# Performance work log

Measured on AMD Instinct MI355X. Metric: run time of the kernel, lower is better.

Reference implementation:

```python
import jax, jax.numpy as jnp
import numpy as np

ATT = 32      # att_size per spatial dim (pooled grid is 32x32, N=1024)
HEADS = 8

def _pool_sum(x, out):
    # adaptive max + adaptive avg pool (exact uniform windows since W%out==0)
    B, C, W, H = x.shape
    kw, kh = W // out, H // out
    r = x.reshape(B, C, out, kw, out, kh)
    return r.max(axis=(3, 5)) + r.mean(axis=(3, 5))

def _lerp_axis(x, out_len, axis):
    in_len = x.shape[axis]
    pos = jnp.arange(out_len, dtype=x.dtype) * ((in_len - 1) / (out_len - 1))
    i0 = jnp.floor(pos).astype(jnp.int32)
    i1 = jnp.minimum(i0 + 1, in_len - 1)
    t = pos - i0.astype(x.dtype)
    shp = [1] * x.ndim
    shp[axis] = out_len
    t = t.reshape(shp)
    return jnp.take(x, i0, axis=axis) * (1 - t) + jnp.take(x, i1, axis=axis) * t

def _upsample_bilinear_ac(x, out_h, out_w):
    # bilinear, align_corners=True (separable)
    return _lerp_axis(_lerp_axis(x, out_h, 2), out_w, 3)

def setup_inputs() -> dict:
    key = jax.random.key(0)
    k1, k2, k3, k4 = jax.random.split(key, 4)
    B, C, W, H = 8, 256, 128, 128
    input1 = jax.random.normal(k1, (B, C, W, H), dtype=jnp.float32)
    input2 = jax.random.normal(k2, (B, C // 2, W, H), dtype=jnp.float32)
    # 1x1 conv: out=C, in=C//2 (kaiming-ish scale)
    conv_w = jax.random.normal(k3, (C, C // 2), dtype=jnp.float32) * (1.0 / np.sqrt(C // 2))
    conv_b = jax.random.normal(k4, (C,), dtype=jnp.float32) * 0.01
    return {"input1": input1, "input2": input2, "conv_w": conv_w, "conv_b": conv_b}

def reference(input1, input2, conv_w, conv_b):
    B, C, W, H = input1.shape
    # channel projection (1x1 conv) since input2 has C//2 channels
    x2 = jnp.einsum('bihw,oi->bohw', input2, conv_w) + conv_b[None, :, None, None]
    p1 = _pool_sum(input1, ATT)   # [B,C,32,32]
    p2 = _pool_sum(x2, ATT)
    N = ATT * ATT
    q = p1.reshape(B, C, N).transpose(2, 0, 1)  # [N,B,C]
    k = p2.reshape(B, C, N).transpose(2, 0, 1)
    v = k
    scale = 1.0 / np.sqrt(C // HEADS)
    w = jnp.einsum('nbc,nec->nbe', q, k)        # [N,B,B]
    w = jax.nn.softmax(w * scale, axis=-1)
    a = jnp.einsum('nbe,nec->nbc', w, v)        # [N,B,C]
    attn = a.transpose(1, 2, 0).reshape(B, C, ATT, ATT)
    up = _upsample_bilinear_ac(attn, W, H)
    return jax.nn.sigmoid(up)
```

## Files before the change

kernel.cpp:

```cpp
#include <hip/hip_runtime.h>
#include <math.h>

namespace {

constexpr int Bn = 8, Cn = 256, CIN = 128, Wd = 128, Hd = 128, ATTn = 32, Nn = ATTn * ATTn;

typedef __attribute__((ext_vector_type(8))) short short8;
typedef __attribute__((ext_vector_type(4))) float f32x4;

__device__ inline unsigned short bf16_rne(float f) {
    unsigned int u = __float_as_uint(f);
    unsigned int r = (u + 0x7FFFu + ((u >> 16) & 1u)) >> 16;
    return (unsigned short)r;
}

__device__ inline int fsw(int px) { return (px ^ (px >> 3)) & 7; }

__global__ __launch_bounds__(256) void pool1_kernel(const float* __restrict__ in1,
                                                    float* __restrict__ p1t) {
    __shared__ float tile[32 * 9];
    const int t = threadIdx.x;
    const int bid = blockIdx.x;
    const int cg = bid & 31, oy = (bid >> 5) & 31, b = bid >> 10;
    const int c = t >> 5, ox = t & 31;

    const float* src = in1 + (((size_t)(b * Cn + cg * 8 + c) * Wd) + oy * 4) * Hd + ox * 4;
    f32x4 r0 = *reinterpret_cast<const f32x4*>(src);
    f32x4 r1 = *reinterpret_cast<const f32x4*>(src + Hd);
    f32x4 r2 = *reinterpret_cast<const f32x4*>(src + 2 * Hd);
    f32x4 r3 = *reinterpret_cast<const f32x4*>(src + 3 * Hd);

    float mx = fmaxf(fmaxf(fmaxf(r0[0], r0[1]), fmaxf(r0[2], r0[3])),
                     fmaxf(fmaxf(r1[0], r1[1]), fmaxf(r1[2], r1[3])));
    mx = fmaxf(mx, fmaxf(fmaxf(fmaxf(r2[0], r2[1]), fmaxf(r2[2], r2[3])),
                         fmaxf(fmaxf(r3[0], r3[1]), fmaxf(r3[2], r3[3]))));
    float sm = ((r0[0] + r0[1]) + (r0[2] + r0[3])) + ((r1[0] + r1[1]) + (r1[2] + r1[3]))
             + ((r2[0] + r2[1]) + (r2[2] + r2[3])) + ((r3[0] + r3[1]) + (r3[2] + r3[3]));

    tile[ox * 9 + c] = mx + sm * (1.f / 16.f);
    __syncthreads();

    const int ox2 = t >> 3, c2 = t & 7;
    p1t[((size_t)b * Nn + oy * 32 + ox2) * Cn + cg * 8 + c2] = tile[ox2 * 9 + c2];
}

__global__ __launch_bounds__(512, 4) void convpool_kernel(const float* __restrict__ in2,
                                                          const float* __restrict__ cw,
                                                          const float* __restrict__ cb,
                                                          float* __restrict__ p2t) {
    __shared__ __align__(16) unsigned char smem[32768];

    const int t = threadIdx.x;
    const int w = t >> 6;
    const int l = t & 63;
    const int bid2 = blockIdx.x;
    const int b = bid2 >> 7;
    const int r = bid2 & 127;
    const int oy = r >> 2, xq = r & 3;

    f32x4 ra[2][4];
    int x4v[2], rowv[2], k4v[2];
#pragma unroll
    for (int h = 0; h < 2; ++h) {
        const int i = t + h * 512;
        x4v[h] = i & 7; rowv[h] = (i >> 3) & 3; k4v[h] = i >> 5;
        const float* p = in2 + ((size_t)(b * CIN + k4v[h] * 4) * Wd + oy * 4 + rowv[h]) * Hd
                         + xq * 32 + x4v[h] * 4;
#pragma unroll
        for (int kk2 = 0; kk2 < 4; ++kk2)
            ra[h][kk2] = *reinterpret_cast<const f32x4*>(p + (size_t)kk2 * Wd * Hd);
    }

    const int n_lo = l & 15;
    const int khi = l >> 4;
    short8 bfrag[2][4];
#pragma unroll
    for (int f = 0; f < 2; ++f) {
        const int n = w * 32 + f * 16 + n_lo;
#pragma unroll
        for (int kk = 0; kk < 4; ++kk) {
            const float* wp = cw + n * CIN + kk * 32 + khi * 8;
            f32x4 va = *reinterpret_cast<const f32x4*>(wp);
            f32x4 vb = *reinterpret_cast<const f32x4*>(wp + 4);
            short8 s;
            s[0] = (short)bf16_rne(va[0]); s[1] = (short)bf16_rne(va[1]);
            s[2] = (short)bf16_rne(va[2]); s[3] = (short)bf16_rne(va[3]);
            s[4] = (short)bf16_rne(vb[0]); s[5] = (short)bf16_rne(vb[1]);
            s[6] = (short)bf16_rne(vb[2]); s[7] = (short)bf16_rne(vb[3]);
            bfrag[f][kk] = s;
        }
    }
    const float bias2_0 = 2.f * cb[w * 32 + n_lo];
    const float bias2_1 = 2.f * cb[w * 32 + 16 + n_lo];

#pragma unroll
    for (int h = 0; h < 2; ++h) {
#pragma unroll
        for (int j = 0; j < 4; ++j) {
            const int px = x4v[h] * 16 + rowv[h] * 4 + j;
            uint2 u;
            u.x = (unsigned int)bf16_rne(ra[h][0][j]) | ((unsigned int)bf16_rne(ra[h][1][j]) << 16);
            u.y = (unsigned int)bf16_rne(ra[h][2][j]) | ((unsigned int)bf16_rne(ra[h][3][j]) << 16);
            const int off = px * 256 + ((k4v[h] * 8) ^ (fsw(px) << 4));
            *reinterpret_cast<uint2*>(smem + off) = u;
        }
    }
    __syncthreads();

#pragma unroll
    for (int cl = 0; cl < 8; ++cl) {
        f32x4 acc0 = {0.f, 0.f, 0.f, 0.f};
        f32x4 acc1 = {0.f, 0.f, 0.f, 0.f};
        const int px = cl * 16 + n_lo;
        const int sw = fsw(px) << 4;
#pragma unroll
        for (int kk = 0; kk < 4; ++kk) {
            short8 a = *reinterpret_cast<const short8*>(
                smem + px * 256 + ((kk * 64 + khi * 16) ^ sw));
            acc0 = __builtin_amdgcn_mfma_f32_16x16x32_bf16(a, bfrag[0][kk], acc0, 0, 0, 0);
            acc1 = __builtin_amdgcn_mfma_f32_16x16x32_bf16(a, bfrag[1][kk], acc1, 0, 0, 0);
        }
        float mx0 = fmaxf(fmaxf(acc0[0], acc0[1]), fmaxf(acc0[2], acc0[3]));
        float sm0 = (acc0[0] + acc0[1]) + (acc0[2] + acc0[3]);
        float mx1 = fmaxf(fmaxf(acc1[0], acc1[1]), fmaxf(acc1[2], acc1[3]));
        float sm1 = (acc1[0] + acc1[1]) + (acc1[2] + acc1[3]);
        mx0 = fmaxf(mx0, __shfl_xor(mx0, 16)); sm0 += __shfl_xor(sm0, 16);
        mx0 = fmaxf(mx0, __shfl_xor(mx0, 32)); sm0 += __shfl_xor(sm0, 32);
        mx1 = fmaxf(mx1, __shfl_xor(mx1, 16)); sm1 += __shfl_xor(sm1, 16);
        mx1 = fmaxf(mx1, __shfl_xor(mx1, 32)); sm1 += __shfl_xor(sm1, 32);
        if (l < 16) {
            const int cell = oy * 32 + xq * 8 + cl;
            float* dst = p2t + ((size_t)b * Nn + cell) * Cn + w * 32 + n_lo;
            dst[0]  = mx0 + sm0 * (1.f / 16.f) + bias2_0;
            dst[16] = mx1 + sm1 * (1.f / 16.f) + bias2_1;
        }
    }
}

__global__ __launch_bounds__(256) void attn_kernel(const float* __restrict__ p1t,
                                                   const float* __restrict__ p2t,
                                                   float* __restrict__ att) {
    __shared__ float q[Bn][260];
    __shared__ float kk[Bn][260];
    __shared__ float wsm[Bn][8];
    const int n = blockIdx.x, t = threadIdx.x;

#pragma unroll
    for (int i = 0; i < 2; ++i) {
        const int f = t + i * 256;
        const int bb = f >> 6, cq = f & 63;
        const size_t off = ((size_t)bb * Nn + n) * Cn + cq * 4;
        *reinterpret_cast<float4*>(&q[bb][cq * 4])  = *reinterpret_cast<const float4*>(p1t + off);
        *reinterpret_cast<float4*>(&kk[bb][cq * 4]) = *reinterpret_cast<const float4*>(p2t + off);
    }
    __syncthreads();

    {
        const int chunk = t & 3, pair = t >> 2;
        const int e = pair & 7, bb = pair >> 3;
        float s = 0.f;
#pragma unroll
        for (int i = 0; i < 64; ++i)
            s = fmaf(q[bb][i * 4 + chunk], kk[e][i * 4 + chunk], s);
        s += __shfl_xor(s, 1);
        s += __shfl_xor(s, 2);
        s *= 0.17677669529663687f;
        float m = fmaxf(s, __shfl_xor(s, 4));
        m = fmaxf(m, __shfl_xor(m, 8));
        m = fmaxf(m, __shfl_xor(m, 16));
        float p = __expf(s - m);
        float d = p + __shfl_xor(p, 4);
        d += __shfl_xor(d, 8);
        d += __shfl_xor(d, 16);
        if (chunk == 0) wsm[bb][e] = p / d;
    }
    __syncthreads();

    float kv[8];
#pragma unroll
    for (int e = 0; e < 8; ++e) kv[e] = kk[e][t];
#pragma unroll
    for (int bb = 0; bb < 8; ++bb) {
        float s = 0.f;
#pragma unroll
        for (int e = 0; e < 8; ++e) s = fmaf(wsm[bb][e], kv[e], s);
        att[((size_t)bb * Cn + t) * Nn + n] = s;
    }
}

__global__ __launch_bounds__(256) void upsample_kernel(const float* __restrict__ att,
                                                       float* __restrict__ out) {
    __shared__ float tile[ATTn * ATTn];
    int bc = blockIdx.x, t = threadIdx.x;
    reinterpret_cast<float4*>(tile)[t] =
        reinterpret_cast<const float4*>(att + (size_t)bc * Nn)[t];
    __syncthreads();

    int tx = t & 31, ty = t >> 5;
    int xi0[4], xi1[4];
    float xt[4];
#pragma unroll
    for (int j = 0; j < 4; ++j) {
        int x = tx * 4 + j;
        float pos = (float)x * (31.f / 127.f);
        int i0 = (int)pos;
        xi0[j] = i0;
        xi1[j] = min(i0 + 1, 31);
        xt[j] = pos - (float)i0;
    }

    for (int r = 0; r < 16; ++r) {
        int y = ty + r * 8;
        float posy = (float)y * (31.f / 127.f);
        int y0 = (int)posy;
        int y1 = min(y0 + 1, 31);
        float ft = posy - (float)y0;
        float o_[4];
#pragma unroll
        for (int j = 0; j < 4; ++j) {
            float v00 = tile[y0 * 32 + xi0[j]];
            float v01 = tile[y0 * 32 + xi1[j]];
            float v10 = tile[y1 * 32 + xi0[j]];
            float v11 = tile[y1 * 32 + xi1[j]];
            float top = v00 * (1.f - ft) + v10 * ft;
            float bot = v01 * (1.f - ft) + v11 * ft;
            float val = top * (1.f - xt[j]) + bot * xt[j];
            o_[j] = 1.f / (1.f + __expf(-val));
        }
        *reinterpret_cast<float4*>(out + ((size_t)bc * Wd + y) * Hd + tx * 4) =
            make_float4(o_[0], o_[1], o_[2], o_[3]);
    }
}

}

extern "C" void kernel_launch(void* const* d_in, const int* in_sizes, int n_in,
                              void* d_out, int out_size, void* d_ws, size_t ws_size,
                              hipStream_t stream) {
    const float* input1 = (const float*)d_in[0];
    const float* input2 = (const float*)d_in[1];
    const float* conv_w = (const float*)d_in[2];
    const float* conv_b = (const float*)d_in[3];
    float* out = (float*)d_out;

    float* p1t = (float*)d_ws;
    float* p2t = p1t + (size_t)Bn * Cn * Nn;
    float* att = p2t + (size_t)Bn * Cn * Nn;

    pool1_kernel<<<dim3(8192), dim3(256), 0, stream>>>(input1, p1t);
    convpool_kernel<<<dim3(1024), dim3(512), 0, stream>>>(input2, conv_w, conv_b, p2t);
    attn_kernel<<<dim3(Nn), dim3(256), 0, stream>>>(p1t, p2t, att);
    upsample_kernel<<<dim3(Bn * Cn), dim3(256), 0, stream>>>(att, out);
}
```

Measured before the change: 112.3 us.

## Restructure pooling kernels for larger per-block tiles and coalesced output stores

The first pooling kernel now has each block handle a quarter of an image for 8 channels. It reads contiguous rows with full float4 coalescing, reduces with shuffles and a small shared scratch, and writes 8 channels per pixel as two vector stores. The conv+pool kernel now processes a full 32-cell output row per block in two half-row passes with 64KB LDS, accumulating the max/sum partials in registers. It stages the output in LDS so the p2t writes are fully coalesced. Grid sizes drop to 1024 and 256 blocks, which risks lower occupancy and less latency hiding. The extra __syncthreads in the per-channel loop of the first kernel add overhead.

```diff
diff --git a/kernel.cpp b/kernel.cpp
--- a/kernel.cpp
+++ b/kernel.cpp
@@ -18,61 +18,84 @@
 
 __global__ __launch_bounds__(256) void pool1_kernel(const float* __restrict__ in1,
                                                     float* __restrict__ p1t) {
-    __shared__ float tile[32 * 9];
+    __shared__ float2 scratch[8][2][32];
     const int t = threadIdx.x;
     const int bid = blockIdx.x;
-    const int cg = bid & 31, oy = (bid >> 5) & 31, b = bid >> 10;
-    const int c = t >> 5, ox = t & 31;
-
-    const float* src = in1 + (((size_t)(b * Cn + cg * 8 + c) * Wd) + oy * 4) * Hd + ox * 4;
-    f32x4 r0 = *reinterpret_cast<const f32x4*>(src);
-    f32x4 r1 = *reinterpret_cast<const f32x4*>(src + Hd);
-    f32x4 r2 = *reinterpret_cast<const f32x4*>(src + 2 * Hd);
-    f32x4 r3 = *reinterpret_cast<const f32x4*>(src + 3 * Hd);
-
-    float mx = fmaxf(fmaxf(fmaxf(r0[0], r0[1]), fmaxf(r0[2], r0[3])),
-                     fmaxf(fmaxf(r1[0], r1[1]), fmaxf(r1[2], r1[3])));
-    mx = fmaxf(mx, fmaxf(fmaxf(fmaxf(r2[0], r2[1]), fmaxf(r2[2], r2[3])),
-                         fmaxf(fmaxf(r3[0], r3[1]), fmaxf(r3[2], r3[3]))));
-    float sm = ((r0[0] + r0[1]) + (r0[2] + r0[3])) + ((r1[0] + r1[1]) + (r1[2] + r1[3]))
-             + ((r2[0] + r2[1]) + (r2[2] + r2[3])) + ((r3[0] + r3[1]) + (r3[2] + r3[3]));
-
-    tile[ox * 9 + c] = mx + sm * (1.f / 16.f);
-    __syncthreads();
-
-    const int ox2 = t >> 3, c2 = t & 7;
-    p1t[((size_t)b * Nn + oy * 32 + ox2) * Cn + cg * 8 + c2] = tile[ox2 * 9 + c2];
-}
-
-__global__ __launch_bounds__(512, 4) void convpool_kernel(const float* __restrict__ in2,
-                                                          const float* __restrict__ cw,
-                                                          const float* __restrict__ cb,
-                                                          float* __restrict__ p2t) {
-    __shared__ __align__(16) unsigned char smem[32768];
-
-    const int t = threadIdx.x;
-    const int w = t >> 6;
-    const int l = t & 63;
-    const int bid2 = blockIdx.x;
-    const int b = bid2 >> 7;
-    const int r = bid2 & 127;
-    const int oy = r >> 2, xq = r & 3;
-
-    f32x4 ra[2][4];
-    int x4v[2], rowv[2], k4v[2];
-#pragma unroll
-    for (int h = 0; h < 2; ++h) {
-        const int i = t + h * 512;
-        x4v[h] = i & 7; rowv[h] = (i >> 3) & 3; k4v[h] = i >> 5;
-        const float* p = in2 + ((size_t)(b * CIN + k4v[h] * 4) * Wd + oy * 4 + rowv[h]) * Hd
-                         + xq * 32 + x4v[h] * 4;
-#pragma unroll
-        for (int kk2 = 0; kk2 < 4; ++kk2)
-            ra[h][kk2] = *reinterpret_cast<const f32x4*>(p + (size_t)kk2 * Wd * Hd);
-    }
-
-    const int n_lo = l & 15;
-    const int khi = l >> 4;
+    const int b = bid >> 7, cg = (bid >> 2) & 31, yq = bid & 3;
+    const int wx = t & 31;
+    const int pair = (t >> 6) & 1;
+    const int hi = t >> 7;
+
+    float res[8];
+#pragma unroll
+    for (int c = 0; c < 8; ++c) {
+        const float* src = in1 + ((size_t)(b * Cn + cg * 8 + c) << 14) + yq * 4096;
+#pragma unroll
+        for (int i = 0; i < 4; ++i) {
+            f32x4 v = *reinterpret_cast<const f32x4*>(src + i * 1024 + t * 4);
+            float m = fmaxf(fmaxf(v[0], v[1]), fmaxf(v[2], v[3]));
+            float s = (v[0] + v[1]) + (v[2] + v[3]);
+            m = fmaxf(m, __shfl_xor(m, 32));
+            s += __shfl_xor(s, 32);
+            if ((t & 63) < 32) scratch[i * 2 + hi][pair][wx] = make_float2(m, s);
+        }
+        __syncthreads();
+        float2 f0 = scratch[t >> 5][0][wx];
+        float2 f1 = scratch[t >> 5][1][wx];
+        res[c] = fmaxf(f0.x, f1.x) + (f0.y + f1.y) * (1.f / 16.f);
+        __syncthreads();
+    }
+    float* dst = p1t + ((size_t)b * Nn + yq * 256 + t) * Cn + cg * 8;
+    f32x4 o0 = {res[0], res[1], res[2], res[3]};
+    f32x4 o1 = {res[4], res[5], res[6], res[7]};
+    *reinterpret_cast<f32x4*>(dst) = o0;
+    *reinterpret_cast<f32x4*>(dst + 4) = o1;
+}
+
+__global__ __launch_bounds__(512) void convpool_kernel(const float* __restrict__ in2,
+                                                       const float* __restrict__ cw,
+                                                       const float* __restrict__ cb,
+                                                       float* __restrict__ p2t) {
+    __shared__ __align__(16) unsigned char smem[65536];
+
+    const int t = threadIdx.x, w = t >> 6, l = t & 63;
+    const int b = blockIdx.x >> 5, oy = blockIdx.x & 31;
+    const int n_lo = l & 15, khi = l >> 4;
+    const int kq0 = w * 16;
+
+    f32x4 rs0[4][4], rs1[4][4];
+#pragma unroll
+    for (int q = 0; q < 4; ++q)
+#pragma unroll
+        for (int kk = 0; kk < 4; ++kk)
+            rs0[q][kk] = *reinterpret_cast<const f32x4*>(
+                in2 + (size_t)(b * CIN + kq0 + q * 4 + kk) * (Wd * Hd) + (oy * 4) * Hd + l * 4);
+
+#define CWRITE(RS, S)                                                              \
+    {                                                                              \
+        _Pragma("unroll") for (int q = 0; q < 4; ++q) {                            \
+            _Pragma("unroll") for (int i = 0; i < 4; ++i) {                        \
+                uint2 u;                                                           \
+                u.x = (unsigned int)bf16_rne(RS[q][0][i]) |                        \
+                      ((unsigned int)bf16_rne(RS[q][1][i]) << 16);                 \
+                u.y = (unsigned int)bf16_rne(RS[q][2][i]) |                        \
+                      ((unsigned int)bf16_rne(RS[q][3][i]) << 16);                 \
+                const int px2 = (l & 31) * 8 + (l >> 5) * 4 + i;                   \
+                const int byte = px2 * 256 + (((kq0 + q * 4) * 2) ^ (fsw(px2) << 4)); \
+                *reinterpret_cast<uint2*>(smem + byte) = u;                        \
+            }                                                                      \
+        }                                                                          \
+    }
+
+    CWRITE(rs0, 0)
+
+#pragma unroll
+    for (int q = 0; q < 4; ++q)
+#pragma unroll
+        for (int kk = 0; kk < 4; ++kk)
+            rs1[q][kk] = *reinterpret_cast<const f32x4*>(
+                in2 + (size_t)(b * CIN + kq0 + q * 4 + kk) * (Wd * Hd) + (oy * 4 + 2) * Hd + l * 4);
+
     short8 bfrag[2][4];
 #pragma unroll
     for (int f = 0; f < 2; ++f) {
@@ -93,48 +116,62 @@
     const float bias2_0 = 2.f * cb[w * 32 + n_lo];
     const float bias2_1 = 2.f * cb[w * 32 + 16 + n_lo];
 
-#pragma unroll
-    for (int h = 0; h < 2; ++h) {
-#pragma unroll
-        for (int j = 0; j < 4; ++j) {
-            const int px = x4v[h] * 16 + rowv[h] * 4 + j;
-            uint2 u;
-            u.x = (unsigned int)bf16_rne(ra[h][0][j]) | ((unsigned int)bf16_rne(ra[h][1][j]) << 16);
-            u.y = (unsigned int)bf16_rne(ra[h][2][j]) | ((unsigned int)bf16_rne(ra[h][3][j]) << 16);
-            const int off = px * 256 + ((k4v[h] * 8) ^ (fsw(px) << 4));
-            *reinterpret_cast<uint2*>(smem + off) = u;
-        }
-    }
-    __syncthreads();
-
-#pragma unroll
-    for (int cl = 0; cl < 8; ++cl) {
-        f32x4 acc0 = {0.f, 0.f, 0.f, 0.f};
-        f32x4 acc1 = {0.f, 0.f, 0.f, 0.f};
-        const int px = cl * 16 + n_lo;
-        const int sw = fsw(px) << 4;
-#pragma unroll
-        for (int kk = 0; kk < 4; ++kk) {
-            short8 a = *reinterpret_cast<const short8*>(
-                smem + px * 256 + ((kk * 64 + khi * 16) ^ sw));
-            acc0 = __builtin_amdgcn_mfma_f32_16x16x32_bf16(a, bfrag[0][kk], acc0, 0, 0, 0);
-            acc1 = __builtin_amdgcn_mfma_f32_16x16x32_bf16(a, bfrag[1][kk], acc1, 0, 0, 0);
-        }
-        float mx0 = fmaxf(fmaxf(acc0[0], acc0[1]), fmaxf(acc0[2], acc0[3]));
-        float sm0 = (acc0[0] + acc0[1]) + (acc0[2] + acc0[3]);
-        float mx1 = fmaxf(fmaxf(acc1[0], acc1[1]), fmaxf(acc1[2], acc1[3]));
-        float sm1 = (acc1[0] + acc1[1]) + (acc1[2] + acc1[3]);
-        mx0 = fmaxf(mx0, __shfl_xor(mx0, 16)); sm0 += __shfl_xor(sm0, 16);
-        mx0 = fmaxf(mx0, __shfl_xor(mx0, 32)); sm0 += __shfl_xor(sm0, 32);
-        mx1 = fmaxf(mx1, __shfl_xor(mx1, 16)); sm1 += __shfl_xor(sm1, 16);
-        mx1 = fmaxf(mx1, __shfl_xor(mx1, 32)); sm1 += __shfl_xor(sm1, 32);
-        if (l < 16) {
-            const int cell = oy * 32 + xq * 8 + cl;
-            float* dst = p2t + ((size_t)b * Nn + cell) * Cn + w * 32 + n_lo;
-            dst[0]  = mx0 + sm0 * (1.f / 16.f) + bias2_0;
-            dst[16] = mx1 + sm1 * (1.f / 16.f) + bias2_1;
-        }
-    }
+    float PM0[16], PS0[16], PM1[16], PS1[16];
+
+#define COMPUTE(S)                                                                 \
+    {                                                                              \
+        _Pragma("unroll") for (int tau = 0; tau < 16; ++tau) {                     \
+            f32x4 acc0 = {0.f, 0.f, 0.f, 0.f};                                     \
+            f32x4 acc1 = {0.f, 0.f, 0.f, 0.f};                                     \
+            const int px2 = tau * 16 + n_lo;                                       \
+            const int sw = fsw(px2) << 4;                                          \
+            _Pragma("unroll") for (int kk = 0; kk < 4; ++kk) {                     \
+                short8 a = *reinterpret_cast<const short8*>(                       \
+                    smem + px2 * 256 + ((kk * 64 + khi * 16) ^ sw));               \
+                acc0 = __builtin_amdgcn_mfma_f32_16x16x32_bf16(a, bfrag[0][kk], acc0, 0, 0, 0); \
+                acc1 = __builtin_amdgcn_mfma_f32_16x16x32_bf16(a, bfrag[1][kk], acc1, 0, 0, 0); \
+            }                                                                      \
+            float pm0 = fmaxf(fmaxf(acc0[0], acc0[1]), fmaxf(acc0[2], acc0[3]));   \
+            float ps0 = (acc0[0] + acc0[1]) + (acc0[2] + acc0[3]);                 \
+            float pm1 = fmaxf(fmaxf(acc1[0], acc1[1]), fmaxf(acc1[2], acc1[3]));   \
+            float ps1 = (acc1[0] + acc1[1]) + (acc1[2] + acc1[3]);                 \
+            pm0 = fmaxf(pm0, __shfl_xor(pm0, 16)); ps0 += __shfl_xor(ps0, 16);     \
+            pm1 = fmaxf(pm1, __shfl_xor(pm1, 16)); ps1 += __shfl_xor(ps1, 16);     \
+            if (S == 0) {                                                          \
+                PM0[tau] = pm0; PS0[tau] = ps0; PM1[tau] = pm1; PS1[tau] = ps1;    \
+            } else {                                                               \
+                PM0[tau] = fmaxf(PM0[tau], pm0); PS0[tau] += ps0;                  \
+                PM1[tau] = fmaxf(PM1[tau], pm1); PS1[tau] += ps1;                  \
+            }                                                                      \
+        }                                                                          \
+    }
+
+    __syncthreads();
+    COMPUTE(0)
+    __syncthreads();
+    CWRITE(rs1, 1)
+    __syncthreads();
+    COMPUTE(1)
+    __syncthreads();
+
+    float* outl = reinterpret_cast<float*>(smem);
+    if ((khi & 1) == 0) {
+#pragma unroll
+        for (int tau = 0; tau < 16; ++tau) {
+            const int cell = tau * 2 + (khi >> 1);
+            outl[cell * 256 + w * 32 + n_lo]      = PM0[tau] + PS0[tau] * (1.f / 16.f) + bias2_0;
+            outl[cell * 256 + w * 32 + 16 + n_lo] = PM1[tau] + PS1[tau] * (1.f / 16.f) + bias2_1;
+        }
+    }
+    __syncthreads();
+
+    float* dst = p2t + ((size_t)b * Nn + oy * 32) * Cn;
+#pragma unroll
+    for (int j = 0; j < 4; ++j)
+        *reinterpret_cast<f32x4*>(dst + (j * 512 + t) * 4) =
+            *reinterpret_cast<const f32x4*>(outl + (j * 512 + t) * 4);
+#undef CWRITE
+#undef COMPUTE
 }
 
 __global__ __launch_bounds__(256) void attn_kernel(const float* __restrict__ p1t,
@@ -247,8 +284,8 @@
     float* p2t = p1t + (size_t)Bn * Cn * Nn;
     float* att = p2t + (size_t)Bn * Cn * Nn;
 
-    pool1_kernel<<<dim3(8192), dim3(256), 0, stream>>>(input1, p1t);
-    convpool_kernel<<<dim3(1024), dim3(512), 0, stream>>>(input2, conv_w, conv_b, p2t);
+    pool1_kernel<<<dim3(1024), dim3(256), 0, stream>>>(input1, p1t);
+    convpool_kernel<<<dim3(256), dim3(512), 0, stream>>>(input2, conv_w, conv_b, p2t);
     attn_kernel<<<dim3(Nn), dim3(256), 0, stream>>>(p1t, p2t, att);
     upsample_kernel<<<dim3(Bn * Cn), dim3(256), 0, stream>>>(att, out);
 }
```

After: 139.0 us. 1.24x slower.

## Restructure pool1 into persistent blocks with contiguous float4 loads and shuffle reduction

Applied to the files above, without the earlier changes.

The input1 pooling kernel now runs 2048 blocks, each looping over 16 iterations. In each iteration a block reads 1024 contiguous floats as fully coalesced float4 loads, instead of four strided rows per thread. Partial max/sum values are combined across rows with a cross-lane shuffle and then through LDS, and 64 threads write the pooled values. The aim is better load coalescing and fewer blocks. The cost is that stores into p1t become strided by Cn (poorly coalesced writes), and each iteration adds two barriers with only a quarter of the threads active in the final step.

```diff
diff --git a/kernel.cpp b/kernel.cpp
--- a/kernel.cpp
+++ b/kernel.cpp
@@ -18,30 +18,33 @@
 
 __global__ __launch_bounds__(256) void pool1_kernel(const float* __restrict__ in1,
                                                     float* __restrict__ p1t) {
-    __shared__ float tile[32 * 9];
+    __shared__ float2 lds[4][32];
     const int t = threadIdx.x;
-    const int bid = blockIdx.x;
-    const int cg = bid & 31, oy = (bid >> 5) & 31, b = bid >> 10;
-    const int c = t >> 5, ox = t & 31;
-
-    const float* src = in1 + (((size_t)(b * Cn + cg * 8 + c) * Wd) + oy * 4) * Hd + ox * 4;
-    f32x4 r0 = *reinterpret_cast<const f32x4*>(src);
-    f32x4 r1 = *reinterpret_cast<const f32x4*>(src + Hd);
-    f32x4 r2 = *reinterpret_cast<const f32x4*>(src + 2 * Hd);
-    f32x4 r3 = *reinterpret_cast<const f32x4*>(src + 3 * Hd);
-
-    float mx = fmaxf(fmaxf(fmaxf(r0[0], r0[1]), fmaxf(r0[2], r0[3])),
-                     fmaxf(fmaxf(r1[0], r1[1]), fmaxf(r1[2], r1[3])));
-    mx = fmaxf(mx, fmaxf(fmaxf(fmaxf(r2[0], r2[1]), fmaxf(r2[2], r2[3])),
-                         fmaxf(fmaxf(r3[0], r3[1]), fmaxf(r3[2], r3[3]))));
-    float sm = ((r0[0] + r0[1]) + (r0[2] + r0[3])) + ((r1[0] + r1[1]) + (r1[2] + r1[3]))
-             + ((r2[0] + r2[1]) + (r2[2] + r2[3])) + ((r3[0] + r3[1]) + (r3[2] + r3[3]));
-
-    tile[ox * 9 + c] = mx + sm * (1.f / 16.f);
-    __syncthreads();
-
-    const int ox2 = t >> 3, c2 = t & 7;
-    p1t[((size_t)b * Nn + oy * 32 + ox2) * Cn + cg * 8 + c2] = tile[ox2 * 9 + c2];
+    const int ox = t & 31;
+
+#pragma unroll 1
+    for (int iter = 0; iter < 16; ++iter) {
+        const size_t f0 = (size_t)iter * 524288 + (size_t)blockIdx.x * 256;
+        f32x4 v = *reinterpret_cast<const f32x4*>(in1 + ((f0 + t) << 2));
+        float m = fmaxf(fmaxf(v[0], v[1]), fmaxf(v[2], v[3]));
+        float s = (v[0] + v[1]) + (v[2] + v[3]);
+        m = fmaxf(m, __shfl_xor(m, 32));
+        s += __shfl_xor(s, 32);
+        if ((t & 63) < 32) lds[t >> 6][ox] = make_float2(m, s);
+        __syncthreads();
+        if (t < 64) {
+            const int wnd = t >> 5;
+            float2 a  = lds[wnd * 2][t & 31];
+            float2 b2 = lds[wnd * 2 + 1][t & 31];
+            const float r = fmaxf(a.x, b2.x) + (a.y + b2.y) * (1.f / 16.f);
+            const int c   = (int)((f0 >> 12) & 255);
+            const int b   = (int)(f0 >> 20);
+            const int oy0 = (int)((f0 >> 7) & 31);
+            const int n = (oy0 + wnd) * 32 + (t & 31);
+            p1t[((size_t)b * Nn + n) * Cn + c] = r;
+        }
+        __syncthreads();
+    }
 }
 
 __global__ __launch_bounds__(512, 4) void convpool_kernel(const float* __restrict__ in2,
@@ -247,7 +250,7 @@
     float* p2t = p1t + (size_t)Bn * Cn * Nn;
     float* att = p2t + (size_t)Bn * Cn * Nn;
 
-    pool1_kernel<<<dim3(8192), dim3(256), 0, stream>>>(input1, p1t);
+    pool1_kernel<<<dim3(2048), dim3(256), 0, stream>>>(input1, p1t);
     convpool_kernel<<<dim3(1024), dim3(512), 0, stream>>>(input2, conv_w, conv_b, p2t);
     attn_kernel<<<dim3(Nn), dim3(256), 0, stream>>>(p1t, p2t, att);
     upsample_kernel<<<dim3(Bn * Cn), dim3(256), 0, stream>>>(att, out);
```

Result: slower. 116.7 us (+3.9%).
